# Kernel tuning notes

Hardware: AMD Instinct MI355X
Metric: run time of the kernel (lower is better)

The kernel has to match this reference:

```python
import jax
import jax.numpy as jnp
import numpy as np
from jax import lax

DIM = 48
HIDDEN = int(DIM * 2.66)  # 127, matches torch int(dim*ffn_expansion_factor)
EPS_LN = 1e-5
EPS_NORM = 1e-12


def conv2d(x, w, groups=1):
    # x: NCHW, w: OIHW, stride 1, SAME padding (all kernels here are 1x1 or 3x3 pad=1)
    return lax.conv_general_dilated(
        x, w, window_strides=(1, 1), padding='SAME',
        feature_group_count=groups,
        dimension_numbers=('NCHW', 'OIHW', 'NCHW'))


def layernorm_cbias(x, w, b):
    # Restormer WithBias_LayerNorm: normalize over channel dim (biased var)
    mu = jnp.mean(x, axis=1, keepdims=True)
    var = jnp.mean(jnp.square(x - mu), axis=1, keepdims=True)
    xn = (x - mu) * lax.rsqrt(var + EPS_LN)
    return xn * w[None, :, None, None] + b[None, :, None, None]


def l2norm_last(x):
    # torch F.normalize(dim=-1, eps=1e-12)
    n = jnp.sqrt(jnp.sum(jnp.square(x), axis=-1, keepdims=True))
    return x / jnp.maximum(n, EPS_NORM)


def setup_inputs() -> dict:
    key = jax.random.key(0)
    ks = jax.random.split(key, 16)
    s = 0.05
    B, H, W = 2, 512, 512
    return {
        'x': jax.random.normal(ks[0], (B, 3, H, W), dtype=jnp.float32),
        # OverlapPatchEmbed: Conv2d(3, 48, 3, pad=1, bias=False)
        'pe_w': jax.random.normal(ks[1], (DIM, 3, 3, 3), dtype=jnp.float32) * s,
        # norm1 (WithBias)
        'n1_w': jnp.ones((DIM,), dtype=jnp.float32),
        'n1_b': jnp.zeros((DIM,), dtype=jnp.float32),
        # MDTA attention, num_heads=1
        'temp': jnp.ones((1, 1, 1), dtype=jnp.float32),
        'qkv_w': jax.random.normal(ks[2], (DIM * 3, DIM, 1, 1), dtype=jnp.float32) * s,
        'qkv_dw_w': jax.random.normal(ks[3], (DIM * 3, 1, 3, 3), dtype=jnp.float32) * s,
        'po_w': jax.random.normal(ks[4], (DIM, DIM, 1, 1), dtype=jnp.float32) * s,
        # norm2
        'n2_w': jnp.ones((DIM,), dtype=jnp.float32),
        'n2_b': jnp.zeros((DIM,), dtype=jnp.float32),
        # GDFN
        'pi_w': jax.random.normal(ks[5], (HIDDEN * 2, DIM, 1, 1), dtype=jnp.float32) * s,
        'ffn_dw_w': jax.random.normal(ks[6], (HIDDEN * 2, 1, 3, 3), dtype=jnp.float32) * s,
        'fo_w': jax.random.normal(ks[7], (DIM, HIDDEN, 1, 1), dtype=jnp.float32) * s,
    }


def reference(x, pe_w, n1_w, n1_b, temp, qkv_w, qkv_dw_w, po_w, n2_w, n2_b, pi_w, ffn_dw_w, fo_w):
    # Patch embed
    patch = conv2d(x, pe_w)  # [B, 48, H, W]
    B, C, H, W = patch.shape

    # ---- MDTA channel attention on norm1(patch) ----
    y = layernorm_cbias(patch, n1_w, n1_b)
    qkv = conv2d(conv2d(y, qkv_w), qkv_dw_w, groups=3 * C)  # [B, 3C, H, W]
    q, k, v = jnp.split(qkv, 3, axis=1)
    # heads=1: rearrange to [B, C, H*W]
    q = l2norm_last(q.reshape(B, C, H * W))
    k = l2norm_last(k.reshape(B, C, H * W))
    v = v.reshape(B, C, H * W)
    attn = jax.nn.softmax(jnp.einsum('bcn,bdn->bcd', q, k) * temp[0, 0, 0], axis=-1)  # [B, C, C]
    out = jnp.einsum('bcd,bdn->bcn', attn, v).reshape(B, C, H, W)
    attn_out = conv2d(out, po_w)
    first = patch + attn_out

    # ---- GDFN on norm2(first) ----
    y2 = layernorm_cbias(first, n2_w, n2_b)
    h = conv2d(conv2d(y2, pi_w), ffn_dw_w, groups=2 * HIDDEN)  # [B, 254, H, W]
    x1, x2 = jnp.split(h, 2, axis=1)
    ffn = conv2d(jax.nn.gelu(x1, approximate=False) * x2, fo_w)
    return first + ffn  # second_residual [B, 48, H, W]
```

## Files before the change

kernel.cpp:

```cpp
#include <hip/hip_runtime.h>
#include <hip/hip_bf16.h>
#include <math.h>

#define HW 512
#define NPIX (HW*HW)

typedef __hip_bfloat16 bf16;
typedef __attribute__((ext_vector_type(8))) unsigned short u16x8;
typedef __attribute__((ext_vector_type(8))) short s16x8;
typedef __attribute__((ext_vector_type(4))) float f32x4;

__device__ __forceinline__ float b2f(bf16 v) { return __bfloat162float(v); }
__device__ __forceinline__ bf16 f2b(float v) { return __float2bfloat16(v); }

union fu { float f; unsigned int u; };
union bu { bf16 b; unsigned short u; };

__device__ __forceinline__ void ld_bf8(const bf16* p, float* f) {
    u16x8 u = *(const u16x8*)p;
#pragma unroll
    for (int j = 0; j < 8; j++) { fu c; c.u = ((unsigned int)u[j]) << 16; f[j] = c.f; }
}

__device__ __forceinline__ void st_bf8(bf16* p, const float* f) {
    u16x8 u;
#pragma unroll
    for (int j = 0; j < 8; j++) { bu c; c.b = f2b(f[j]); u[j] = c.u; }
    *(u16x8*)p = u;
}

__global__ __launch_bounds__(256) void k_prep(const float* __restrict__ qkvw,
                                              const float* __restrict__ piw,
                                              const float* __restrict__ fow,
                                              bf16* __restrict__ WQ,
                                              bf16* __restrict__ WP,
                                              bf16* __restrict__ WF,
                                              float* __restrict__ Z0,
                                              float* __restrict__ Z1)
{
    int idx = blockIdx.x*256 + threadIdx.x;
    if (idx < 9216) {
        int oc = idx >> 6, k = idx & 63;
        WQ[idx] = f2b(k < 48 ? qkvw[oc*48 + k] : 0.f);
    } else if (idx < 25600) {
        int j = idx - 9216; int oc = j >> 6, k = j & 63;
        WP[j] = f2b((oc < 254 && k < 48) ? piw[oc*48 + k] : 0.f);
    } else if (idx < 31744) {
        int j = idx - 25600; int oc = j >> 7, k = j & 127;
        WF[j] = f2b(k < 127 ? fow[oc*127 + k] : 0.f);
    } else if (idx < 36544) {
        int j = idx - 31744;
        if (j < 2400) Z0[j] = 0.f; else Z1[j-2400] = 0.f;
    }
}

__global__ __launch_bounds__(256) void k_pe(const float* __restrict__ x,
                                            const float* __restrict__ w,
                                            bf16* __restrict__ out)
{
    __shared__ float ws[48*27];
    for (int i = threadIdx.x; i < 48*27; i += 256) ws[i] = w[i];
    __syncthreads();
    int lane = threadIdx.x & 63, wv = threadIdx.x >> 6;
    int row = blockIdx.x*4 + wv;
    int col = lane*8;
    float a[3][3][8];
    float lf[3][3], rt[3][3];
#pragma unroll
    for (int c = 0; c < 3; c++)
#pragma unroll
        for (int r = 0; r < 3; r++) {
            int rr = row + r - 1;
            if (rr >= 0 && rr < HW) {
                const float* p = x + (size_t)c*NPIX + rr*HW + col;
                float4 u0 = *(const float4*)p, u1 = *(const float4*)(p+4);
                a[c][r][0]=u0.x; a[c][r][1]=u0.y; a[c][r][2]=u0.z; a[c][r][3]=u0.w;
                a[c][r][4]=u1.x; a[c][r][5]=u1.y; a[c][r][6]=u1.z; a[c][r][7]=u1.w;
            } else {
#pragma unroll
                for (int j = 0; j < 8; j++) a[c][r][j] = 0.f;
            }
            float l = __shfl_up(a[c][r][7], 1);  lf[c][r] = (lane==0)  ? 0.f : l;
            float rv= __shfl_down(a[c][r][0],1); rt[c][r] = (lane==63) ? 0.f : rv;
        }
    for (int oc = 0; oc < 48; oc++) {
        float acc[8];
#pragma unroll
        for (int j = 0; j < 8; j++) acc[j] = 0.f;
#pragma unroll
        for (int c = 0; c < 3; c++)
#pragma unroll
            for (int r = 0; r < 3; r++) {
                float w0 = ws[oc*27 + c*9 + r*3 + 0];
                float w1 = ws[oc*27 + c*9 + r*3 + 1];
                float w2 = ws[oc*27 + c*9 + r*3 + 2];
#pragma unroll
                for (int j = 0; j < 8; j++) {
                    float xm = (j==0) ? lf[c][r] : a[c][r][j-1];
                    float x0 = a[c][r][j];
                    float xp = (j==7) ? rt[c][r] : a[c][r][j+1];
                    acc[j] += w0*xm + w1*x0 + w2*xp;
                }
            }
        st_bf8(out + (size_t)oc*NPIX + row*HW + col, acc);
    }
}

template<int OC_PAD, int OC_REAL, int MT_PER_WAVE>
__global__ __launch_bounds__(256) void k_ln_mm_mfma(const bf16* __restrict__ in,
                                                    const float* __restrict__ lnw,
                                                    const float* __restrict__ lnb,
                                                    const s16x8* __restrict__ wpad,
                                                    bf16* __restrict__ out)
{
    constexpr int NMT = OC_PAD/16;
    __shared__ s16x8 y_lds[256*8];
    __shared__ float lw[48], lb[48];
    int t = threadIdx.x;
    if (t < 48) { lw[t] = lnw[t]; lb[t] = lnb[t]; }
    int base = blockIdx.x*256;
    int px = base + t;
    float y[48];
    float mu = 0.f;
#pragma unroll
    for (int i = 0; i < 48; i++) { y[i] = b2f(in[(size_t)i*NPIX + px]); mu += y[i]; }
    mu *= (1.f/48.f);
    float var = 0.f;
#pragma unroll
    for (int i = 0; i < 48; i++) { float d = y[i]-mu; var += d*d; }
    float s = rsqrtf(var*(1.f/48.f) + 1e-5f);
    __syncthreads();
#pragma unroll
    for (int i = 0; i < 48; i++) y[i] = (y[i]-mu)*s*lw[i] + lb[i];
#pragma unroll
    for (int kb = 0; kb < 8; kb++) {
        union { s16x8 v; unsigned short us[8]; } pk;
#pragma unroll
        for (int j = 0; j < 8; j++) {
            int c = kb*8 + j;
            bu b; b.b = f2b(c < 48 ? y[c] : 0.f);
            pk.us[j] = (c < 48) ? b.u : (unsigned short)0;
        }
        y_lds[t*8 + (kb ^ (t & 7))] = pk.v;
    }
    __syncthreads();

    int lane = t & 63, wv = t >> 6;
    int q = lane >> 4, n = lane & 15;
    s16x8 a[MT_PER_WAVE][2];
#pragma unroll
    for (int mi = 0; mi < MT_PER_WAVE; mi++) {
        int mt = wv + 4*mi;
        if (mt < NMT) {
            int oc = mt*16 + n;
            a[mi][0] = wpad[oc*8 + q];
            a[mi][1] = wpad[oc*8 + 4 + q];
        }
    }
#pragma unroll 1
    for (int nt = 0; nt < 16; nt++) {
        int npx = nt*16 + n;
        s16x8 b0 = y_lds[npx*8 + (q ^ (npx & 7))];
        s16x8 b1 = y_lds[npx*8 + ((4 + q) ^ (npx & 7))];
        size_t pxg = base + npx;
#pragma unroll
        for (int mi = 0; mi < MT_PER_WAVE; mi++) {
            int mt = wv + 4*mi;
            if (mt >= NMT) continue;
            f32x4 acc = {0.f, 0.f, 0.f, 0.f};
            acc = __builtin_amdgcn_mfma_f32_16x16x32_bf16(a[mi][0], b0, acc, 0, 0, 0);
            acc = __builtin_amdgcn_mfma_f32_16x16x32_bf16(a[mi][1], b1, acc, 0, 0, 0);
            int ocb = mt*16 + q*4;
#pragma unroll
            for (int r = 0; r < 4; r++) {
                int oc = ocb + r;
                if (OC_REAL == OC_PAD || oc < OC_REAL)
                    out[(size_t)oc*NPIX + pxg] = f2b(acc[r]);
            }
        }
    }
}

__global__ __launch_bounds__(256) void k_dw(const bf16* __restrict__ in,
                                            const float* __restrict__ w,
                                            bf16* __restrict__ out)
{
    int ch = blockIdx.y;
    int lane = threadIdx.x & 63, wv = threadIdx.x >> 6;
    int row0 = blockIdx.x*32 + wv*8;
    int col = lane*8;
    const bf16* ip = in + (size_t)ch*NPIX;
    bf16* op = out + (size_t)ch*NPIX;
    float wk[9];
#pragma unroll
    for (int i = 0; i < 9; i++) wk[i] = w[ch*9+i];
    float a[3][8];
    float lf[3], rt[3];

    auto loadrow = [&](int s, int rr) {
        if (rr >= 0 && rr < HW) ld_bf8(ip + rr*HW + col, a[s]);
        else {
#pragma unroll
            for (int j = 0; j < 8; j++) a[s][j] = 0.f;
        }
        float l = __shfl_up(a[s][7], 1);  lf[s] = (lane==0)  ? 0.f : l;
        float rv= __shfl_down(a[s][0],1); rt[s] = (lane==63) ? 0.f : rv;
    };
    loadrow(0, row0-1);
    loadrow(1, row0);
#pragma unroll
    for (int r = 0; r < 8; r++) {
        loadrow((r+2)%3, row0 + r + 1);
        const int s0 = r%3, s1 = (r+1)%3, s2 = (r+2)%3;
        float o[8];
#pragma unroll
        for (int j = 0; j < 8; j++) {
            float sm = 0.f;
#pragma unroll
            for (int kr = 0; kr < 3; kr++) {
                const int ss = (kr==0) ? s0 : (kr==1) ? s1 : s2;
                float xm = (j==0) ? lf[ss] : a[ss][j-1];
                float x0 = a[ss][j];
                float xp = (j==7) ? rt[ss] : a[ss][j+1];
                sm += wk[kr*3+0]*xm + wk[kr*3+1]*x0 + wk[kr*3+2]*xp;
            }
            o[j] = sm;
        }
        st_bf8(op + (row0 + r)*HW + col, o);
    }
}

__global__ __launch_bounds__(512) void k_qkt(const bf16* __restrict__ qm,
                                             const bf16* __restrict__ km,
                                             float* __restrict__ S,
                                             float* __restrict__ sumsq)
{
    __shared__ float Sp[8][48][52];
    __shared__ float ssp[8][96];
    int t = threadIdx.x;
    int lane = t & 63, wv = t >> 6;
    int qg = lane >> 4, n = lane & 15;
    size_t px0 = (size_t)(blockIdx.x*8 + wv) * 128 + qg*8;

    f32x4 acc[3][3];
#pragma unroll
    for (int i = 0; i < 3; i++)
#pragma unroll
        for (int j = 0; j < 3; j++) acc[i][j] = (f32x4){0.f, 0.f, 0.f, 0.f};
    float sq[3] = {0.f, 0.f, 0.f}, sk[3] = {0.f, 0.f, 0.f};

#pragma unroll 2
    for (int s = 0; s < 4; s++) {
        size_t p = px0 + s*32;
        s16x8 qa[3], ka[3];
#pragma unroll
        for (int i = 0; i < 3; i++) {
            qa[i] = *(const s16x8*)&qm[(size_t)(16*i + n)*NPIX + p];
            ka[i] = *(const s16x8*)&km[(size_t)(16*i + n)*NPIX + p];
        }
#pragma unroll
        for (int i = 0; i < 3; i++)
#pragma unroll
            for (int j = 0; j < 3; j++)
                acc[i][j] = __builtin_amdgcn_mfma_f32_16x16x32_bf16(qa[i], ka[j], acc[i][j], 0, 0, 0);
#pragma unroll
        for (int i = 0; i < 3; i++) {
            union { s16x8 v; unsigned short us[8]; } uq, uk;
            uq.v = qa[i]; uk.v = ka[i];
#pragma unroll
            for (int j = 0; j < 8; j++) {
                fu cq; cq.u = ((unsigned int)uq.us[j]) << 16; sq[i] += cq.f*cq.f;
                fu ck; ck.u = ((unsigned int)uk.us[j]) << 16; sk[i] += ck.f*ck.f;
            }
        }
    }

#pragma unroll
    for (int i = 0; i < 3; i++)
#pragma unroll
        for (int j = 0; j < 3; j++)
#pragma unroll
            for (int r = 0; r < 4; r++)
                Sp[wv][16*i + qg*4 + r][16*j + n] = acc[i][j][r];
#pragma unroll
    for (int i = 0; i < 3; i++) {
        float a = sq[i], b = sk[i];
        a += __shfl_down(a, 32); a += __shfl_down(a, 16);
        b += __shfl_down(b, 32); b += __shfl_down(b, 16);
        if (lane < 16) { ssp[wv][16*i + lane] = a; ssp[wv][48 + 16*i + lane] = b; }
    }
    __syncthreads();

    for (int idx = t; idx < 2304; idx += 512) {
        int r = idx / 48, c = idx - r*48;
        float v = 0.f;
#pragma unroll
        for (int w = 0; w < 8; w++) v += Sp[w][r][c];
        atomicAdd(&S[idx], v);
    }
    if (t < 96) {
        float v = 0.f;
#pragma unroll
        for (int w = 0; w < 8; w++) v += ssp[w][t];
        atomicAdd(&sumsq[t], v);
    }
}

__global__ __launch_bounds__(256) void k_attn_final(const float* __restrict__ S,
                                                    const float* __restrict__ sumsq,
                                                    const float* __restrict__ po_w,
                                                    const float* __restrict__ temp,
                                                    float* __restrict__ M)
{
    __shared__ float attn[48][48];
    __shared__ float nrm[96];
    int t = threadIdx.x;
    if (t < 96) nrm[t] = fmaxf(sqrtf(sumsq[t]), 1e-12f);
    __syncthreads();
    float tmp = temp[0];
    if (t < 48) {
        float row[48];
        float mx = -1e30f;
#pragma unroll
        for (int d = 0; d < 48; d++) {
            float l = S[t*48+d] / (nrm[t]*nrm[48+d]) * tmp;
            row[d] = l; mx = fmaxf(mx, l);
        }
        float sum = 0.f;
#pragma unroll
        for (int d = 0; d < 48; d++) { float e = expf(row[d]-mx); sum += e; row[d] = e; }
        float inv = 1.f/sum;
#pragma unroll
        for (int d = 0; d < 48; d++) attn[t][d] = row[d]*inv;
    }
    __syncthreads();
    for (int idx = t; idx < 2304; idx += 256) {
        int cp = idx/48, d = idx%48;
        float acc = 0.f;
#pragma unroll
        for (int c = 0; c < 48; c++) acc += po_w[cp*48+c] * attn[c][d];
        M[idx] = acc;
    }
}

__global__ __launch_bounds__(256) void k_attnv_ln_mm(const bf16* __restrict__ v,
                                                     const float* __restrict__ M,
                                                     bf16* __restrict__ patch,
                                                     const float* __restrict__ lnw,
                                                     const float* __restrict__ lnb,
                                                     const s16x8* __restrict__ wpad,
                                                     bf16* __restrict__ out)
{
    constexpr int OC_REAL = 254;
    __shared__ s16x8 y_lds[256*8];
    __shared__ float lw[48], lb[48];
    int t = threadIdx.x;
    if (t < 48) { lw[t] = lnw[t]; lb[t] = lnb[t]; }
    int base = blockIdx.x*256;
    int px = base + t;

    float vv[48];
#pragma unroll
    for (int i = 0; i < 48; i++) vv[i] = b2f(v[(size_t)i*NPIX + px]);
    float y[48];
    float mu = 0.f;
#pragma unroll 4
    for (int oc = 0; oc < 48; oc++) {
        const float4* mr = (const float4*)(M + oc*48);
        float acc = 0.f;
#pragma unroll
        for (int i = 0; i < 12; i++) {
            float4 m4 = mr[i];
            acc += m4.x*vv[4*i] + m4.y*vv[4*i+1] + m4.z*vv[4*i+2] + m4.w*vv[4*i+3];
        }
        size_t gidx = (size_t)oc*NPIX + px;
        bf16 fb = f2b(b2f(patch[gidx]) + acc);
        patch[gidx] = fb;
        float fv = b2f(fb);
        y[oc] = fv; mu += fv;
    }

    mu *= (1.f/48.f);
    float var = 0.f;
#pragma unroll
    for (int i = 0; i < 48; i++) { float d = y[i]-mu; var += d*d; }
    float s = rsqrtf(var*(1.f/48.f) + 1e-5f);
    __syncthreads();
#pragma unroll
    for (int i = 0; i < 48; i++) y[i] = (y[i]-mu)*s*lw[i] + lb[i];
#pragma unroll
    for (int kb = 0; kb < 8; kb++) {
        union { s16x8 v; unsigned short us[8]; } pk;
#pragma unroll
        for (int j = 0; j < 8; j++) {
            int c = kb*8 + j;
            bu b; b.b = f2b(c < 48 ? y[c] : 0.f);
            pk.us[j] = (c < 48) ? b.u : (unsigned short)0;
        }
        y_lds[t*8 + (kb ^ (t & 7))] = pk.v;
    }
    __syncthreads();

    int lane = t & 63, wv = t >> 6;
    int q = lane >> 4, n = lane & 15;
    s16x8 a[4][2];
#pragma unroll
    for (int mi = 0; mi < 4; mi++) {
        int oc = (wv + 4*mi)*16 + n;
        a[mi][0] = wpad[oc*8 + q];
        a[mi][1] = wpad[oc*8 + 4 + q];
    }
#pragma unroll 1
    for (int nt = 0; nt < 16; nt++) {
        int npx = nt*16 + n;
        s16x8 b0 = y_lds[npx*8 + (q ^ (npx & 7))];
        s16x8 b1 = y_lds[npx*8 + ((4 + q) ^ (npx & 7))];
        size_t pxg = base + npx;
#pragma unroll
        for (int mi = 0; mi < 4; mi++) {
            int mt = wv + 4*mi;
            f32x4 acc = {0.f, 0.f, 0.f, 0.f};
            acc = __builtin_amdgcn_mfma_f32_16x16x32_bf16(a[mi][0], b0, acc, 0, 0, 0);
            acc = __builtin_amdgcn_mfma_f32_16x16x32_bf16(a[mi][1], b1, acc, 0, 0, 0);
            int ocb = mt*16 + q*4;
#pragma unroll
            for (int r = 0; r < 4; r++) {
                int oc = ocb + r;
                if (oc < OC_REAL)
                    out[(size_t)oc*NPIX + pxg] = f2b(acc[r]);
            }
        }
    }
}

__global__ __launch_bounds__(256) void k_dw_glu(const bf16* __restrict__ h1,
                                                const float* __restrict__ w,
                                                bf16* __restrict__ g)
{
    int ch = blockIdx.y;
    int lane = threadIdx.x & 63, wv = threadIdx.x >> 6;
    int row0 = blockIdx.x*32 + wv*8;
    int col = lane*8;
    float w1[9], w2[9];
#pragma unroll
    for (int i = 0; i < 9; i++) { w1[i] = w[ch*9+i]; w2[i] = w[(ch+127)*9+i]; }
    const bf16* i1 = h1 + (size_t)ch*NPIX;
    const bf16* i2 = h1 + (size_t)(ch+127)*NPIX;
    bf16* op = g + (size_t)ch*NPIX;
    float aa[3][8], bb[3][8];
    float lfa[3], rta[3], lfb[3], rtb[3];

    auto loadrow = [&](int s, int rr) {
        if (rr >= 0 && rr < HW) {
            ld_bf8(i1 + rr*HW + col, aa[s]);
            ld_bf8(i2 + rr*HW + col, bb[s]);
        } else {
#pragma unroll
            for (int j = 0; j < 8; j++) { aa[s][j] = 0.f; bb[s][j] = 0.f; }
        }
        float l1 = __shfl_up(aa[s][7],1);   lfa[s] = (lane==0)  ? 0.f : l1;
        float r1 = __shfl_down(aa[s][0],1); rta[s] = (lane==63) ? 0.f : r1;
        float l2 = __shfl_up(bb[s][7],1);   lfb[s] = (lane==0)  ? 0.f : l2;
        float r2 = __shfl_down(bb[s][0],1); rtb[s] = (lane==63) ? 0.f : r2;
    };
    loadrow(0, row0-1);
    loadrow(1, row0);
#pragma unroll
    for (int r = 0; r < 8; r++) {
        loadrow((r+2)%3, row0 + r + 1);
        const int s0 = r%3, s1 = (r+1)%3, s2 = (r+2)%3;
        float o[8];
#pragma unroll
        for (int j = 0; j < 8; j++) {
            float sum1 = 0.f, sum2 = 0.f;
#pragma unroll
            for (int kr = 0; kr < 3; kr++) {
                const int ss = (kr==0) ? s0 : (kr==1) ? s1 : s2;
                float xm = (j==0) ? lfa[ss] : aa[ss][j-1];
                float x0 = aa[ss][j];
                float xp = (j==7) ? rta[ss] : aa[ss][j+1];
                sum1 += w1[kr*3+0]*xm + w1[kr*3+1]*x0 + w1[kr*3+2]*xp;
                float ym = (j==0) ? lfb[ss] : bb[ss][j-1];
                float y0 = bb[ss][j];
                float yp = (j==7) ? rtb[ss] : bb[ss][j+1];
                sum2 += w2[kr*3+0]*ym + w2[kr*3+1]*y0 + w2[kr*3+2]*yp;
            }
            float ge = 0.5f*sum1*(1.f + erff(sum1*0.70710678118654752f));
            o[j] = ge*sum2;
        }
        st_bf8(op + (row0 + r)*HW + col, o);
    }
}

__global__ __launch_bounds__(256) void k_fo_mfma(const bf16* __restrict__ g,
                                                 const s16x8* __restrict__ wfo,
                                                 const bf16* __restrict__ first,
                                                 float* __restrict__ out)
{
    __shared__ s16x8 glds[256*16];
    int t = threadIdx.x;
    int base = blockIdx.x*256;
    int px = base + t;
#pragma unroll
    for (int kb = 0; kb < 16; kb++) {
        union { s16x8 v; unsigned short us[8]; } pk;
#pragma unroll
        for (int j = 0; j < 8; j++) {
            int c = kb*8 + j;
            if (c < 127) { bu b; b.b = g[(size_t)c*NPIX + px]; pk.us[j] = b.u; }
            else pk.us[j] = 0;
        }
        glds[t*16 + (kb ^ (t & 15))] = pk.v;
    }
    __syncthreads();
    int lane = t & 63, wv = t >> 6;
    int q = lane >> 4, n = lane & 15;
    s16x8 a[3][4];
#pragma unroll
    for (int mt = 0; mt < 3; mt++) {
        int oc = mt*16 + n;
#pragma unroll
        for (int kc = 0; kc < 4; kc++)
            a[mt][kc] = wfo[oc*16 + kc*4 + q];
    }
#pragma unroll 1
    for (int ni = 0; ni < 4; ni++) {
        int nt = wv*4 + ni;
        int npx = nt*16 + n;
        s16x8 b[4];
#pragma unroll
        for (int kc = 0; kc < 4; kc++)
            b[kc] = glds[npx*16 + ((kc*4 + q) ^ (npx & 15))];
        size_t pxg = base + npx;
#pragma unroll
        for (int mt = 0; mt < 3; mt++) {
            f32x4 acc = {0.f, 0.f, 0.f, 0.f};
#pragma unroll
            for (int kc = 0; kc < 4; kc++)
                acc = __builtin_amdgcn_mfma_f32_16x16x32_bf16(a[mt][kc], b[kc], acc, 0, 0, 0);
            int ocb = mt*16 + q*4;
#pragma unroll
            for (int r = 0; r < 4; r++) {
                int oc = ocb + r;
                out[(size_t)oc*NPIX + pxg] = b2f(first[(size_t)oc*NPIX + pxg]) + acc[r];
            }
        }
    }
}

extern "C" void kernel_launch(void* const* d_in, const int* in_sizes, int n_in,
                              void* d_out, int out_size, void* d_ws, size_t ws_size,
                              hipStream_t stream)
{
    const float* x     = (const float*)d_in[0];
    const float* pe_w  = (const float*)d_in[1];
    const float* n1w   = (const float*)d_in[2];
    const float* n1b   = (const float*)d_in[3];
    const float* temp  = (const float*)d_in[4];
    const float* qkvw  = (const float*)d_in[5];
    const float* qkvdw = (const float*)d_in[6];
    const float* pow_  = (const float*)d_in[7];
    const float* n2w   = (const float*)d_in[8];
    const float* n2b   = (const float*)d_in[9];
    const float* piw   = (const float*)d_in[10];
    const float* ffndw = (const float*)d_in[11];
    const float* fow   = (const float*)d_in[12];
    float* out = (float*)d_out;

    bf16*  Pb = (bf16*)d_ws;
    bf16*  A  = Pb + (size_t)48*NPIX;
    bf16*  Bq = A + (size_t)144*NPIX;
    bf16*  H1 = A;
    bf16*  G  = A + (size_t)254*NPIX;
    bf16*  WQ = A + (size_t)381*NPIX;
    bf16*  WP = WQ + 144*64;
    bf16*  WF = WP + 256*64;
    float* SM0 = (float*)(A + (size_t)384*NPIX);
    float* SM1 = SM0 + 4704;

    dim3 blk(256);
    int nb1 = NPIX/256;
    int nr  = HW/4;
    int nrw = HW/32;

    k_prep<<<dim3(143), blk, 0, stream>>>(qkvw, piw, fow, WQ, WP, WF, SM0, SM1);

    for (int b = 0; b < 2; b++) {
        const float* xb   = x   + (size_t)b*3*NPIX;
        float*       outb = out + (size_t)b*48*NPIX;
        float* SMb   = b ? SM1 : SM0;
        float* sumsq = SMb;
        float* S     = SMb + 96;
        float* M     = SMb + 2400;

        k_pe<<<dim3(nr), blk, 0, stream>>>(xb, pe_w, Pb);
        k_ln_mm_mfma<144,144,3><<<dim3(nb1), blk, 0, stream>>>(Pb, n1w, n1b, (const s16x8*)WQ, A);
        k_dw<<<dim3(nrw, 144), blk, 0, stream>>>(A, qkvdw, Bq);
        k_qkt<<<dim3(NPIX/1024), dim3(512), 0, stream>>>(Bq, Bq + (size_t)48*NPIX, S, sumsq);
        k_attn_final<<<dim3(1), blk, 0, stream>>>(S, sumsq, pow_, temp, M);
        k_attnv_ln_mm<<<dim3(nb1), blk, 0, stream>>>(Bq + (size_t)96*NPIX, M, Pb, n2w, n2b, (const s16x8*)WP, H1);
        k_dw_glu<<<dim3(nrw, 127), blk, 0, stream>>>(H1, ffndw, G);
        k_fo_mfma<<<dim3(nb1), blk, 0, stream>>>(G, (const s16x8*)WF, Pb, outb);
    }
}
```

Baseline: 742.7 us.

## Stage MFMA outputs in LDS for vectorized stores; split attn-v from LN-matmul

The LN+1x1-conv MFMA kernel now writes bf16 results into a shared-memory staging tile and then emits 16-byte vectorized row stores per output channel, replacing scattered 2-byte global stores. The fused attn·v + LN + matmul kernel is split into a separate k_attnv kernel, which processes two pixels per thread with M held in LDS, followed by the generic templated LN-matmul kernel. This trades an extra pass over the 48-channel patch tensor and more LDS use (and lower occupancy) for coalesced output writes on the wide 144- and 254-channel outputs.

```diff
diff --git a/kernel.cpp b/kernel.cpp
--- a/kernel.cpp
+++ b/kernel.cpp
@@ -115,9 +115,8 @@
 {
     constexpr int NMT = OC_PAD/16;
     __shared__ s16x8 y_lds[256*8];
-    __shared__ float lw[48], lb[48];
+    __shared__ unsigned short stage[OC_PAD][72];
     int t = threadIdx.x;
-    if (t < 48) { lw[t] = lnw[t]; lb[t] = lnb[t]; }
     int base = blockIdx.x*256;
     int px = base + t;
     float y[48];
@@ -129,9 +128,8 @@
 #pragma unroll
     for (int i = 0; i < 48; i++) { float d = y[i]-mu; var += d*d; }
     float s = rsqrtf(var*(1.f/48.f) + 1e-5f);
-    __syncthreads();
-#pragma unroll
-    for (int i = 0; i < 48; i++) y[i] = (y[i]-mu)*s*lw[i] + lb[i];
+#pragma unroll
+    for (int i = 0; i < 48; i++) y[i] = (y[i]-mu)*s*lnw[i] + lnb[i];
 #pragma unroll
     for (int kb = 0; kb < 8; kb++) {
         union { s16x8 v; unsigned short us[8]; } pk;
@@ -158,26 +156,38 @@
         }
     }
 #pragma unroll 1
-    for (int nt = 0; nt < 16; nt++) {
-        int npx = nt*16 + n;
-        s16x8 b0 = y_lds[npx*8 + (q ^ (npx & 7))];
-        s16x8 b1 = y_lds[npx*8 + ((4 + q) ^ (npx & 7))];
-        size_t pxg = base + npx;
-#pragma unroll
-        for (int mi = 0; mi < MT_PER_WAVE; mi++) {
-            int mt = wv + 4*mi;
-            if (mt >= NMT) continue;
-            f32x4 acc = {0.f, 0.f, 0.f, 0.f};
-            acc = __builtin_amdgcn_mfma_f32_16x16x32_bf16(a[mi][0], b0, acc, 0, 0, 0);
-            acc = __builtin_amdgcn_mfma_f32_16x16x32_bf16(a[mi][1], b1, acc, 0, 0, 0);
-            int ocb = mt*16 + q*4;
-#pragma unroll
-            for (int r = 0; r < 4; r++) {
-                int oc = ocb + r;
-                if (OC_REAL == OC_PAD || oc < OC_REAL)
-                    out[(size_t)oc*NPIX + pxg] = f2b(acc[r]);
-            }
-        }
+    for (int g = 0; g < 4; g++) {
+#pragma unroll
+        for (int sub = 0; sub < 4; sub++) {
+            int nt = g*4 + sub;
+            int npx = nt*16 + n;
+            s16x8 b0 = y_lds[npx*8 + (q ^ (npx & 7))];
+            s16x8 b1 = y_lds[npx*8 + ((4 + q) ^ (npx & 7))];
+#pragma unroll
+            for (int mi = 0; mi < MT_PER_WAVE; mi++) {
+                int mt = wv + 4*mi;
+                if (mt >= NMT) continue;
+                f32x4 acc = {0.f, 0.f, 0.f, 0.f};
+                acc = __builtin_amdgcn_mfma_f32_16x16x32_bf16(a[mi][0], b0, acc, 0, 0, 0);
+                acc = __builtin_amdgcn_mfma_f32_16x16x32_bf16(a[mi][1], b1, acc, 0, 0, 0);
+                int ocb = mt*16 + q*4;
+#pragma unroll
+                for (int r = 0; r < 4; r++) {
+                    bu bb; bb.b = f2b(acc[r]);
+                    stage[ocb + r][sub*16 + n] = bb.u;
+                }
+            }
+        }
+        __syncthreads();
+        if (t < OC_REAL) {
+            const u16x8* sp = (const u16x8*)stage[t];
+            u16x8 c0 = sp[0], c1 = sp[1], c2 = sp[2], c3 = sp[3];
+            u16x8 c4 = sp[4], c5 = sp[5], c6 = sp[6], c7 = sp[7];
+            u16x8* op = (u16x8*)(out + (size_t)t*NPIX + base + g*64);
+            op[0] = c0; op[1] = c1; op[2] = c2; op[3] = c3;
+            op[4] = c4; op[5] = c5; op[6] = c6; op[7] = c7;
+        }
+        __syncthreads();
     }
 }
 
@@ -343,93 +353,35 @@
     }
 }
 
-__global__ __launch_bounds__(256) void k_attnv_ln_mm(const bf16* __restrict__ v,
-                                                     const float* __restrict__ M,
-                                                     bf16* __restrict__ patch,
-                                                     const float* __restrict__ lnw,
-                                                     const float* __restrict__ lnb,
-                                                     const s16x8* __restrict__ wpad,
-                                                     bf16* __restrict__ out)
-{
-    constexpr int OC_REAL = 254;
-    __shared__ s16x8 y_lds[256*8];
-    __shared__ float lw[48], lb[48];
-    int t = threadIdx.x;
-    if (t < 48) { lw[t] = lnw[t]; lb[t] = lnb[t]; }
-    int base = blockIdx.x*256;
-    int px = base + t;
-
-    float vv[48];
-#pragma unroll
-    for (int i = 0; i < 48; i++) vv[i] = b2f(v[(size_t)i*NPIX + px]);
-    float y[48];
-    float mu = 0.f;
-#pragma unroll 4
+__global__ __launch_bounds__(256) void k_attnv(const bf16* __restrict__ v,
+                                               const float* __restrict__ M,
+                                               bf16* __restrict__ patch)
+{
+    __shared__ float Ms[48*48];
+    for (int i = threadIdx.x; i < 2304; i += 256) Ms[i] = M[i];
+    __syncthreads();
+    int p = (blockIdx.x*256 + threadIdx.x)*2;
+    float v0[48], v1[48];
+#pragma unroll
+    for (int i = 0; i < 48; i++) {
+        unsigned int word = *(const unsigned int*)&v[(size_t)i*NPIX + p];
+        fu c0, c1; c0.u = word << 16; c1.u = word & 0xffff0000u;
+        v0[i] = c0.f; v1[i] = c1.f;
+    }
     for (int oc = 0; oc < 48; oc++) {
-        const float4* mr = (const float4*)(M + oc*48);
-        float acc = 0.f;
+        const float4* wr = (const float4*)&Ms[oc*48];
+        float a0 = 0.f, a1 = 0.f;
 #pragma unroll
         for (int i = 0; i < 12; i++) {
-            float4 m4 = mr[i];
-            acc += m4.x*vv[4*i] + m4.y*vv[4*i+1] + m4.z*vv[4*i+2] + m4.w*vv[4*i+3];
-        }
-        size_t gidx = (size_t)oc*NPIX + px;
-        bf16 fb = f2b(b2f(patch[gidx]) + acc);
-        patch[gidx] = fb;
-        float fv = b2f(fb);
-        y[oc] = fv; mu += fv;
-    }
-
-    mu *= (1.f/48.f);
-    float var = 0.f;
-#pragma unroll
-    for (int i = 0; i < 48; i++) { float d = y[i]-mu; var += d*d; }
-    float s = rsqrtf(var*(1.f/48.f) + 1e-5f);
-    __syncthreads();
-#pragma unroll
-    for (int i = 0; i < 48; i++) y[i] = (y[i]-mu)*s*lw[i] + lb[i];
-#pragma unroll
-    for (int kb = 0; kb < 8; kb++) {
-        union { s16x8 v; unsigned short us[8]; } pk;
-#pragma unroll
-        for (int j = 0; j < 8; j++) {
-            int c = kb*8 + j;
-            bu b; b.b = f2b(c < 48 ? y[c] : 0.f);
-            pk.us[j] = (c < 48) ? b.u : (unsigned short)0;
-        }
-        y_lds[t*8 + (kb ^ (t & 7))] = pk.v;
-    }
-    __syncthreads();
-
-    int lane = t & 63, wv = t >> 6;
-    int q = lane >> 4, n = lane & 15;
-    s16x8 a[4][2];
-#pragma unroll
-    for (int mi = 0; mi < 4; mi++) {
-        int oc = (wv + 4*mi)*16 + n;
-        a[mi][0] = wpad[oc*8 + q];
-        a[mi][1] = wpad[oc*8 + 4 + q];
-    }
-#pragma unroll 1
-    for (int nt = 0; nt < 16; nt++) {
-        int npx = nt*16 + n;
-        s16x8 b0 = y_lds[npx*8 + (q ^ (npx & 7))];
-        s16x8 b1 = y_lds[npx*8 + ((4 + q) ^ (npx & 7))];
-        size_t pxg = base + npx;
-#pragma unroll
-        for (int mi = 0; mi < 4; mi++) {
-            int mt = wv + 4*mi;
-            f32x4 acc = {0.f, 0.f, 0.f, 0.f};
-            acc = __builtin_amdgcn_mfma_f32_16x16x32_bf16(a[mi][0], b0, acc, 0, 0, 0);
-            acc = __builtin_amdgcn_mfma_f32_16x16x32_bf16(a[mi][1], b1, acc, 0, 0, 0);
-            int ocb = mt*16 + q*4;
-#pragma unroll
-            for (int r = 0; r < 4; r++) {
-                int oc = ocb + r;
-                if (oc < OC_REAL)
-                    out[(size_t)oc*NPIX + pxg] = f2b(acc[r]);
-            }
-        }
+            float4 w4 = wr[i];
+            a0 += w4.x*v0[4*i] + w4.y*v0[4*i+1] + w4.z*v0[4*i+2] + w4.w*v0[4*i+3];
+            a1 += w4.x*v1[4*i] + w4.y*v1[4*i+1] + w4.z*v1[4*i+2] + w4.w*v1[4*i+3];
+        }
+        unsigned int* pp = (unsigned int*)&patch[(size_t)oc*NPIX + p];
+        unsigned int old = *pp;
+        fu f0, f1; f0.u = old << 16; f1.u = old & 0xffff0000u;
+        bu b0, b1; b0.b = f2b(f0.f + a0); b1.b = f2b(f1.f + a1);
+        *pp = (unsigned int)b0.u | ((unsigned int)b1.u << 16);
     }
 }
 
@@ -580,6 +532,7 @@
 
     dim3 blk(256);
     int nb1 = NPIX/256;
+    int nb2 = NPIX/512;
     int nr  = HW/4;
     int nrw = HW/32;
 
@@ -598,7 +551,8 @@
         k_dw<<<dim3(nrw, 144), blk, 0, stream>>>(A, qkvdw, Bq);
         k_qkt<<<dim3(NPIX/1024), dim3(512), 0, stream>>>(Bq, Bq + (size_t)48*NPIX, S, sumsq);
         k_attn_final<<<dim3(1), blk, 0, stream>>>(S, sumsq, pow_, temp, M);
-        k_attnv_ln_mm<<<dim3(nb1), blk, 0, stream>>>(Bq + (size_t)96*NPIX, M, Pb, n2w, n2b, (const s16x8*)WP, H1);
+        k_attnv<<<dim3(nb2), blk, 0, stream>>>(Bq + (size_t)96*NPIX, M, Pb);
+        k_ln_mm_mfma<256,254,4><<<dim3(nb1), blk, 0, stream>>>(Pb, n2w, n2b, (const s16x8*)WP, H1);
         k_dw_glu<<<dim3(nrw, 127), blk, 0, stream>>>(H1, ffndw, G);
         k_fo_mfma<<<dim3(nb1), blk, 0, stream>>>(G, (const s16x8*)WF, Pb, outb);
     }
```

After: 727.2 us. 2.1% less time.
